# Performance work log

Hardware: AMD Instinct MI355X
Metric: run time of the kernel (lower is better)

Reference implementation:

```python
import jax, jax.numpy as jnp
import numpy as np

T, B, D, H = 1024, 4, 1024, 16
HD = D // H  # 64


def _layernorm(x, g, b, eps=1e-5):
    mu = jnp.mean(x, axis=-1, keepdims=True)
    var = jnp.var(x, axis=-1, keepdims=True)
    return (x - mu) / jnp.sqrt(var + eps) * g + b


def setup_inputs() -> dict:
    key = jax.random.key(0)
    ks = jax.random.split(key, 16)
    s = 1.0 / np.sqrt(D)
    mk = lambda k: jax.random.uniform(k, (D, D), jnp.float32, -s, s)
    return {
        "x": jax.random.normal(ks[0], (T, B, D), jnp.float32),
        "Wq": mk(ks[1]), "bq": jnp.zeros((D,), jnp.float32),
        "Wk": mk(ks[2]), "bk": jnp.zeros((D,), jnp.float32),
        "Wv": mk(ks[3]), "bv": jnp.zeros((D,), jnp.float32),
        "Wo": mk(ks[4]), "bo": jnp.zeros((D,), jnp.float32),
        "Wl": mk(ks[5]), "bl": jnp.zeros((D,), jnp.float32),
        "g1": jnp.ones((D,), jnp.float32), "b1": jnp.zeros((D,), jnp.float32),
        "g2": jnp.ones((D,), jnp.float32), "b2": jnp.zeros((D,), jnp.float32),
    }


def reference(x, Wq, bq, Wk, bk, Wv, bv, Wo, bo, Wl, bl, g1, b1, g2, b2):
    # x: [T, B, D] (time-major). The torch loop over dim 0 with full keys/values
    # is equivalent to batched full (non-causal) self-attention.
    q = (x @ Wq.T + bq).reshape(T, B, H, HD)
    k = (x @ Wk.T + bk).reshape(T, B, H, HD)
    v = (x @ Wv.T + bv).reshape(T, B, H, HD)
    scores = jnp.einsum("tbhd,sbhd->bhts", q, k) / np.sqrt(HD).astype(np.float32)
    attn = jax.nn.softmax(scores, axis=-1)          # [B,H,T,T]
    ctx = jnp.einsum("bhts,sbhd->tbhd", attn, v).reshape(T, B, D)
    attn_out = ctx @ Wo.T + bo
    # dropout p: identity at inference
    h = _layernorm(attn_out + x, g1, b1)
    ffn = h @ Wl.T + bl
    return _layernorm(ffn + h, g2, b2)
```

## Files before the change

### kernel.cpp

```cpp
#include <hip/hip_runtime.h>

#define T_ 1024
#define B_ 4
#define D_ 1024
#define H_ 16
#define HD_ 64
#define M_ (T_ * B_)

typedef _Float16 f16;
typedef f16 f16x8 __attribute__((ext_vector_type(8)));
typedef f16 f16x4 __attribute__((ext_vector_type(4)));
typedef float f32x4 __attribute__((ext_vector_type(4)));

__device__ __forceinline__ void gl2lds16(const void* g, void* l) {
  __builtin_amdgcn_global_load_lds(
      (const __attribute__((address_space(1))) void*)g,
      (__attribute__((address_space(3))) void*)l, 16, 0, 0);
}

struct Prep {
  const float* x;
  const float* w[5];
  const float* b[3];
  f16* xd;
  f16* wd[5];
  float* bd;
};

__global__ __launch_bounds__(256) void prep(Prep p) {
  const int bid = blockIdx.x, tid = threadIdx.x;
  if (bid < 4096) {
    const int i = bid * 1024 + tid * 4;
    float4 v = *(const float4*)(p.x + i);
    f16x4 o = {(f16)v.x, (f16)v.y, (f16)v.z, (f16)v.w};
    *(f16x4*)(p.xd + i) = o;
  } else if (bid < 9216) {
    const int wi = bid - 4096;
    const int a = wi >> 10;
    const int i = (wi & 1023) * 1024 + tid * 4;
    float4 v = *(const float4*)(p.w[a] + i);
    f16x4 o = {(f16)v.x, (f16)v.y, (f16)v.z, (f16)v.w};
    *(f16x4*)(p.wd[a] + i) = o;
  } else {
    const int j = bid - 9216;
    const int i = tid * 4;
    *(float4*)(p.bd + j * 1024 + i) = *(const float4*)(p.b[j] + i);
  }
}

__global__ __launch_bounds__(256) void gemm_f16(const f16* __restrict__ A,
                                                const f16* __restrict__ W,
                                                const float* __restrict__ bias,
                                                const f16* __restrict__ res,
                                                f16* __restrict__ out) {
  constexpr int K = D_, BK = 32;
  __shared__ __align__(16) f16 As[128 * BK];
  __shared__ __align__(16) f16 Bs[64 * BK];
  const int tid = threadIdx.x;
  const int lane = tid & 63;
  const int quad = lane >> 4, l16 = lane & 15;
  const int m0 = blockIdx.y * 128, n0 = blockIdx.x * 64;
  const int wave = tid >> 6;
  const int wm = (wave >> 1) * 64, wn = (wave & 1) * 32;
  f32x4 acc[4][2] = {};
  for (int kt = 0; kt < K / BK; ++kt) {
    __syncthreads();
    const int kb = kt * BK;
#pragma unroll
    for (int i = 0; i < 2; ++i) {
      const int c = i * 256 + tid;
      const int row = c >> 2, col8 = (c & 3) * 8;
      const int ldsbase = (i * 256 + (tid & ~63)) * 8;
      gl2lds16(A + (size_t)(m0 + row) * K + kb + col8, &As[ldsbase]);
    }
    {
      const int row = tid >> 2, col8 = (tid & 3) * 8;
      const int ldsbase = (tid & ~63) * 8;
      gl2lds16(W + (size_t)(n0 + row) * K + kb + col8, &Bs[ldsbase]);
    }
    __syncthreads();
    f16x8 af[4], bf[2];
#pragma unroll
    for (int i = 0; i < 4; ++i)
      af[i] = *(const f16x8*)&As[(wm + i * 16 + l16) * BK + quad * 8];
#pragma unroll
    for (int j = 0; j < 2; ++j)
      bf[j] = *(const f16x8*)&Bs[(wn + j * 16 + l16) * BK + quad * 8];
#pragma unroll
    for (int i = 0; i < 4; ++i)
#pragma unroll
      for (int j = 0; j < 2; ++j)
        acc[i][j] = __builtin_amdgcn_mfma_f32_16x16x32_f16(af[i], bf[j], acc[i][j], 0, 0, 0);
  }
#pragma unroll
  for (int j = 0; j < 2; ++j) {
    const int n = n0 + wn + j * 16 + l16;
    const float bn = bias[n];
#pragma unroll
    for (int i = 0; i < 4; ++i) {
      const int m = m0 + wm + i * 16 + quad * 4;
#pragma unroll
      for (int r = 0; r < 4; ++r) {
        const float v = acc[i][j][r] + bn + (float)res[(size_t)(m + r) * D_ + n];
        out[(size_t)(m + r) * D_ + n] = (f16)v;
      }
    }
  }
}

#define QSCALE 0.18033688011112042f
__global__ __launch_bounds__(256) void gemm_qkv(const f16* __restrict__ A,
                                                const f16* __restrict__ W,
                                                const float* __restrict__ bias,
                                                f16* __restrict__ qo,
                                                f16* __restrict__ ko,
                                                f16* __restrict__ vo) {
  constexpr int K = D_, BK = 32;
  __shared__ __align__(16) f16 As[128 * BK];
  __shared__ __align__(16) f16 Bs[128 * BK];
  const int tid = threadIdx.x;
  const int lane = tid & 63;
  const int quad = lane >> 4, l16 = lane & 15;
  const int m0 = blockIdx.y * 128, n0 = blockIdx.x * 128;
  const int wave = tid >> 6;
  const int wm = (wave >> 1) * 64, wn = (wave & 1) * 64;
  f32x4 acc[4][4] = {};
  for (int kt = 0; kt < K / BK; ++kt) {
    __syncthreads();
    const int kb = kt * BK;
#pragma unroll
    for (int i = 0; i < 2; ++i) {
      const int c = i * 256 + tid;
      const int row = c >> 2, col8 = (c & 3) * 8;
      const int ldsbase = (i * 256 + (tid & ~63)) * 8;
      gl2lds16(A + (size_t)(m0 + row) * K + kb + col8, &As[ldsbase]);
      gl2lds16(W + (size_t)(n0 + row) * K + kb + col8, &Bs[ldsbase]);
    }
    __syncthreads();
    f16x8 af[4], bf[4];
#pragma unroll
    for (int i = 0; i < 4; ++i)
      af[i] = *(const f16x8*)&As[(wm + i * 16 + l16) * BK + quad * 8];
#pragma unroll
    for (int j = 0; j < 4; ++j)
      bf[j] = *(const f16x8*)&Bs[(wn + j * 16 + l16) * BK + quad * 8];
#pragma unroll
    for (int i = 0; i < 4; ++i)
#pragma unroll
      for (int j = 0; j < 4; ++j)
        acc[i][j] = __builtin_amdgcn_mfma_f32_16x16x32_f16(af[i], bf[j], acc[i][j], 0, 0, 0);
  }
  const int which = n0 >> 10;
  f16* outp = which == 0 ? qo : (which == 1 ? ko : vo);
  const float sc = which == 0 ? QSCALE : 1.0f;
#pragma unroll
  for (int j = 0; j < 4; ++j) {
    const int n = n0 + wn + j * 16 + l16;
    const float bn = bias[n];
    const int nl = n & 1023;
    const int hh = nl >> 6, d = nl & 63;
#pragma unroll
    for (int i = 0; i < 4; ++i) {
#pragma unroll
      for (int r = 0; r < 4; ++r) {
        const int m = m0 + wm + i * 16 + quad * 4 + r;
        const float v = (acc[i][j][r] + bn) * sc;
        const int t = m >> 2, bb = m & 3;
        if (which < 2)
          outp[((size_t)(bb * H_ + hh) * T_ + t) * HD_ + d] = (f16)v;
        else
          outp[((size_t)(bb * H_ + hh) * HD_ + d) * T_ + t] = (f16)v;
      }
    }
  }
}

__global__ __launch_bounds__(256) void attn(const f16* __restrict__ Q,
                                            const f16* __restrict__ Km,
                                            const f16* __restrict__ Vt,
                                            f16* __restrict__ ctx) {
  constexpr int SK = 128;
  constexpr int NT = T_ / SK;
  __shared__ __align__(16) f16 Ks[SK * HD_];
  __shared__ __align__(16) f16 Vs[HD_ * SK];
  __shared__ __align__(16) f16 Ps[4][16 * 36];
  const int tid = threadIdx.x, wave = tid >> 6, lane = tid & 63;
  const int quad = lane >> 4, l16 = lane & 15;
  const int bh = blockIdx.x;
  const int b = bh >> 4, h = bh & 15;
  const int q0 = blockIdx.y * 128;
  const f16* Qbh = Q + ((size_t)bh * T_ + q0 + wave * 32) * HD_;
  const f16* Kbh = Km + (size_t)bh * T_ * HD_;
  const f16* Vbh = Vt + (size_t)bh * HD_ * T_;

  f16x8 qf[2][2];
#pragma unroll
  for (int c = 0; c < 2; ++c) {
    qf[c][0] = *(const f16x8*)&Qbh[(c * 16 + l16) * HD_ + quad * 8];
    qf[c][1] = *(const f16x8*)&Qbh[(c * 16 + l16) * HD_ + 32 + quad * 8];
  }

  const f16* kq[4];
  const f16* vq[4];
  int lds_o[4];
#pragma unroll
  for (int it = 0; it < 4; ++it) {
    const int n = wave * 256 + it * 64 + lane;
    const int s = n >> 3, cp = n & 7, cl = cp ^ (s & 7);
    kq[it] = Kbh + (size_t)s * HD_ + cl * 8;
    const int d = n >> 4, cp2 = n & 15, cl2 = cp2 ^ (d & 7);
    vq[it] = Vbh + (size_t)d * T_ + cl2 * 8;
    lds_o[it] = (wave * 256 + it * 64) * 8;
  }

  f32x4 O[4][2] = {};
  float lsum[2] = {0.f, 0.f};
  const int sw = l16 & 7;

  for (int kt = 0; kt < NT; ++kt) {
    __syncthreads();
#pragma unroll
    for (int it = 0; it < 4; ++it) {
      gl2lds16(kq[it], &Ks[lds_o[it]]);
      kq[it] += SK * HD_;
    }
#pragma unroll
    for (int it = 0; it < 4; ++it) {
      gl2lds16(vq[it], &Vs[lds_o[it]]);
      vq[it] += SK;
    }
    __syncthreads();

    float st[8][2][4];
#pragma unroll
    for (int s = 0; s < 8; ++s) {
      const int row = s * 16 + l16;
      const f16x8 ka = *(const f16x8*)&Ks[row * HD_ + (quad ^ sw) * 8];
      const f16x8 kb = *(const f16x8*)&Ks[row * HD_ + ((4 + quad) ^ sw) * 8];
#pragma unroll
      for (int c = 0; c < 2; ++c) {
        f32x4 a = {};
        a = __builtin_amdgcn_mfma_f32_16x16x32_f16(ka, qf[c][0], a, 0, 0, 0);
        a = __builtin_amdgcn_mfma_f32_16x16x32_f16(kb, qf[c][1], a, 0, 0, 0);
#pragma unroll
        for (int r = 0; r < 4; ++r) {
          st[s][c][r] = exp2f(a[r]);
          lsum[c] += st[s][c][r];
        }
      }
    }

#pragma unroll
    for (int cI = 0; cI < 4; ++cI) {
#pragma unroll
      for (int c = 0; c < 2; ++c) {
        f16* pw = &Ps[wave][0];
        f16x4 w0, w1;
#pragma unroll
        for (int r = 0; r < 4; ++r) {
          w0[r] = (f16)st[2 * cI][c][r];
          w1[r] = (f16)st[2 * cI + 1][c][r];
        }
        *(f16x4*)&pw[l16 * 36 + quad * 4] = w0;
        *(f16x4*)&pw[l16 * 36 + 16 + quad * 4] = w1;
        const f16x8 pf = *(const f16x8*)&pw[l16 * 36 + quad * 8];
#pragma unroll
        for (int dt = 0; dt < 4; ++dt) {
          const int d = dt * 16 + l16;
          const f16x8 vf = *(const f16x8*)&Vs[d * SK + (((cI * 4 + quad) ^ sw) * 8)];
          O[dt][c] = __builtin_amdgcn_mfma_f32_16x16x32_f16(vf, pf, O[dt][c], 0, 0, 0);
        }
      }
    }
  }

#pragma unroll
  for (int c = 0; c < 2; ++c) {
    float l = lsum[c];
    l += __shfl_xor(l, 16, 64);
    l += __shfl_xor(l, 32, 64);
    const float linv = 1.f / l;
    const int t = q0 + wave * 32 + c * 16 + l16;
#pragma unroll
    for (int dt = 0; dt < 4; ++dt) {
      f16x4 ov;
#pragma unroll
      for (int r = 0; r < 4; ++r) ov[r] = (f16)(O[dt][c][r] * linv);
      *(f16x4*)&ctx[((size_t)t * B_ + b) * D_ + h * HD_ + dt * 16 + quad * 4] = ov;
    }
  }
}

__global__ __launch_bounds__(256) void lnorm(const f16* __restrict__ a,
                                             const float* __restrict__ g,
                                             const float* __restrict__ bb,
                                             f16* __restrict__ outh,
                                             float* __restrict__ outf) {
  const int row = blockIdx.x, tid = threadIdx.x;
  const size_t base = (size_t)row * D_;
  f16x4 va = *(const f16x4*)&a[base + tid * 4];
  float x0 = (float)va[0], x1 = (float)va[1], x2 = (float)va[2], x3 = (float)va[3];
  float s = x0 + x1 + x2 + x3;
  float sq = x0 * x0 + x1 * x1 + x2 * x2 + x3 * x3;
#pragma unroll
  for (int off = 32; off; off >>= 1) {
    s += __shfl_down(s, off, 64);
    sq += __shfl_down(sq, off, 64);
  }
  __shared__ float rs[4], rq[4];
  __shared__ float mean_s, rstd_s;
  if ((tid & 63) == 0) { rs[tid >> 6] = s; rq[tid >> 6] = sq; }
  __syncthreads();
  if (tid == 0) {
    float S = rs[0] + rs[1] + rs[2] + rs[3];
    float Qq = rq[0] + rq[1] + rq[2] + rq[3];
    float mean = S / D_;
    float var = Qq / D_ - mean * mean;
    mean_s = mean;
    rstd_s = rsqrtf(var + 1e-5f);
  }
  __syncthreads();
  const float mean = mean_s, rstd = rstd_s;
  float4 vg = *(const float4*)&g[tid * 4];
  float4 vb = *(const float4*)&bb[tid * 4];
  float y0 = (x0 - mean) * rstd * vg.x + vb.x;
  float y1 = (x1 - mean) * rstd * vg.y + vb.y;
  float y2 = (x2 - mean) * rstd * vg.z + vb.z;
  float y3 = (x3 - mean) * rstd * vg.w + vb.w;
  if (outh) {
    f16x4 o = {(f16)y0, (f16)y1, (f16)y2, (f16)y3};
    *(f16x4*)&outh[base + tid * 4] = o;
  }
  if (outf)
    *(float4*)&outf[base + tid * 4] = make_float4(y0, y1, y2, y3);
}

extern "C" void kernel_launch(void* const* d_in, const int* in_sizes, int n_in,
                              void* d_out, int out_size, void* d_ws, size_t ws_size,
                              hipStream_t stream) {
  const float* x  = (const float*)d_in[0];
  const float* Wq = (const float*)d_in[1];
  const float* bq = (const float*)d_in[2];
  const float* Wk = (const float*)d_in[3];
  const float* bk = (const float*)d_in[4];
  const float* Wv = (const float*)d_in[5];
  const float* bv = (const float*)d_in[6];
  const float* Wo = (const float*)d_in[7];
  const float* bo = (const float*)d_in[8];
  const float* Wl = (const float*)d_in[9];
  const float* bl = (const float*)d_in[10];
  const float* g1 = (const float*)d_in[11];
  const float* b1 = (const float*)d_in[12];
  const float* g2 = (const float*)d_in[13];
  const float* b2 = (const float*)d_in[14];

  char* ws = (char*)d_ws;
  const size_t MB = 1 << 20;
  f16*   xb   = (f16*)(ws + 0 * MB);
  f16*   wqkv = (f16*)(ws + 8 * MB);
  f16*   wob  = (f16*)(ws + 14 * MB);
  f16*   wlb  = (f16*)(ws + 16 * MB);
  float* bqkv = (float*)(ws + 18 * MB);
  f16*   qb   = (f16*)(ws + 19 * MB);
  f16*   kb   = (f16*)(ws + 27 * MB);
  f16*   vb   = (f16*)(ws + 35 * MB);
  f16*   ctxb = (f16*)(ws + 43 * MB);
  f16*   att  = qb;
  f16*   hbuf = kb;

  Prep p;
  p.x = x;
  p.w[0] = Wq; p.w[1] = Wk; p.w[2] = Wv; p.w[3] = Wo; p.w[4] = Wl;
  p.b[0] = bq; p.b[1] = bk; p.b[2] = bv;
  p.xd = xb;
  p.wd[0] = wqkv; p.wd[1] = wqkv + D_ * D_; p.wd[2] = wqkv + 2 * D_ * D_;
  p.wd[3] = wob; p.wd[4] = wlb;
  p.bd = bqkv;
  prep<<<9219, 256, 0, stream>>>(p);

  gemm_qkv<<<dim3(3 * D_ / 128, M_ / 128), 256, 0, stream>>>(xb, wqkv, bqkv, qb, kb, vb);

  attn<<<dim3(B_ * H_, T_ / 128), 256, 0, stream>>>(qb, kb, vb, ctxb);

  dim3 gg(D_ / 64, M_ / 128);
  gemm_f16<<<gg, 256, 0, stream>>>(ctxb, wob, bo, xb, att);
  lnorm<<<M_, 256, 0, stream>>>(att, g1, b1, hbuf, nullptr);
  gemm_f16<<<gg, 256, 0, stream>>>(hbuf, wlb, bl, hbuf, att);
  lnorm<<<M_, 256, 0, stream>>>(att, g2, b2, nullptr, (float*)d_out);
}
```

Measured before the change: 238.8 us.

## Fuse all stages into one persistent megakernel with grid-wide barriers

```diff
diff --git a/kernel.cpp b/kernel.cpp
--- a/kernel.cpp
+++ b/kernel.cpp
@@ -6,63 +6,94 @@
 #define H_ 16
 #define HD_ 64
 #define M_ (T_ * B_)
+#define NBLK 512
 
 typedef _Float16 f16;
 typedef f16 f16x8 __attribute__((ext_vector_type(8)));
 typedef f16 f16x4 __attribute__((ext_vector_type(4)));
 typedef float f32x4 __attribute__((ext_vector_type(4)));
 
+#define QSCALE 0.18033688011112042f
+
 __device__ __forceinline__ void gl2lds16(const void* g, void* l) {
   __builtin_amdgcn_global_load_lds(
       (const __attribute__((address_space(1))) void*)g,
       (__attribute__((address_space(3))) void*)l, 16, 0, 0);
 }
 
-struct Prep {
+__device__ __forceinline__ void gbar(unsigned* cnt, unsigned* gen) {
+  __syncthreads();
+  if (threadIdx.x == 0) {
+    unsigned g = __hip_atomic_load(gen, __ATOMIC_RELAXED, __HIP_MEMORY_SCOPE_AGENT);
+    __threadfence();
+    unsigned a = __hip_atomic_fetch_add(cnt, 1u, __ATOMIC_ACQ_REL, __HIP_MEMORY_SCOPE_AGENT);
+    if (a == NBLK - 1) {
+      __hip_atomic_store(cnt, 0u, __ATOMIC_RELAXED, __HIP_MEMORY_SCOPE_AGENT);
+      __hip_atomic_fetch_add(gen, 1u, __ATOMIC_RELEASE, __HIP_MEMORY_SCOPE_AGENT);
+    } else {
+      while (__hip_atomic_load(gen, __ATOMIC_ACQUIRE, __HIP_MEMORY_SCOPE_AGENT) == g)
+        __builtin_amdgcn_s_sleep(2);
+    }
+    __threadfence();
+  }
+  __syncthreads();
+}
+
+struct MegaArgs {
   const float* x;
   const float* w[5];
-  const float* b[3];
-  f16* xd;
+  const float* b3[3];
+  const float* bo;
+  const float* bl;
+  const float *g1, *b1, *g2, *b2;
+  f16* xb;
   f16* wd[5];
-  float* bd;
+  float* bqkv;
+  f16 *qb, *kb, *vb, *ctxb, *att, *hbuf;
+  float* out;
+  unsigned* bar;
 };
 
-__global__ __launch_bounds__(256) void prep(Prep p) {
-  const int bid = blockIdx.x, tid = threadIdx.x;
-  if (bid < 4096) {
-    const int i = bid * 1024 + tid * 4;
-    float4 v = *(const float4*)(p.x + i);
+__device__ __forceinline__ void prep_stage(const MegaArgs& A, int gtid) {
+  constexpr int XCH = 1 << 20;
+  constexpr int WCH = 1 << 18;
+  constexpr int NCH = XCH + 5 * WCH;
+#pragma unroll 1
+  for (int i = gtid; i < NCH; i += NBLK * 256) {
+    const float4* s;
+    f16* d;
+    int off;
+    if (i < XCH) {
+      s = (const float4*)A.x; d = A.xb; off = i;
+    } else {
+      const int wi = i - XCH;
+      const int a = wi >> 18;
+      off = wi & (WCH - 1);
+      s = (const float4*)A.w[a];
+      d = A.wd[a];
+    }
+    float4 v = s[off];
     f16x4 o = {(f16)v.x, (f16)v.y, (f16)v.z, (f16)v.w};
-    *(f16x4*)(p.xd + i) = o;
-  } else if (bid < 9216) {
-    const int wi = bid - 4096;
-    const int a = wi >> 10;
-    const int i = (wi & 1023) * 1024 + tid * 4;
-    float4 v = *(const float4*)(p.w[a] + i);
-    f16x4 o = {(f16)v.x, (f16)v.y, (f16)v.z, (f16)v.w};
-    *(f16x4*)(p.wd[a] + i) = o;
-  } else {
-    const int j = bid - 9216;
-    const int i = tid * 4;
-    *(float4*)(p.bd + j * 1024 + i) = *(const float4*)(p.b[j] + i);
-  }
-}
-
-__global__ __launch_bounds__(256) void gemm_f16(const f16* __restrict__ A,
-                                                const f16* __restrict__ W,
-                                                const float* __restrict__ bias,
-                                                const f16* __restrict__ res,
-                                                f16* __restrict__ out) {
+    *(f16x4*)(d + off * 4) = o;
+  }
+  if (gtid < 768) {
+    const int j = gtid >> 8, t = gtid & 255;
+    ((float4*)(A.bqkv + j * 1024))[t] = ((const float4*)A.b3[j])[t];
+  }
+}
+
+__device__ __forceinline__ void qkv_stage(const MegaArgs& A, char* smem, int vt, int tid) {
   constexpr int K = D_, BK = 32;
-  __shared__ __align__(16) f16 As[128 * BK];
-  __shared__ __align__(16) f16 Bs[64 * BK];
-  const int tid = threadIdx.x;
+  f16* As = (f16*)smem;
+  f16* Bs = (f16*)(smem + 8192);
   const int lane = tid & 63;
   const int quad = lane >> 4, l16 = lane & 15;
-  const int m0 = blockIdx.y * 128, n0 = blockIdx.x * 64;
+  const int m0 = (vt / 24) * 128, n0 = (vt % 24) * 128;
   const int wave = tid >> 6;
-  const int wm = (wave >> 1) * 64, wn = (wave & 1) * 32;
-  f32x4 acc[4][2] = {};
+  const int wm = (wave >> 1) * 64, wn = (wave & 1) * 64;
+  const f16* Ap = A.xb;
+  const f16* Wp = A.wd[0];
+  f32x4 acc[4][4] = {};
   for (int kt = 0; kt < K / BK; ++kt) {
     __syncthreads();
     const int kb = kt * BK;
@@ -71,77 +102,15 @@
       const int c = i * 256 + tid;
       const int row = c >> 2, col8 = (c & 3) * 8;
       const int ldsbase = (i * 256 + (tid & ~63)) * 8;
-      gl2lds16(A + (size_t)(m0 + row) * K + kb + col8, &As[ldsbase]);
-    }
-    {
-      const int row = tid >> 2, col8 = (tid & 3) * 8;
-      const int ldsbase = (tid & ~63) * 8;
-      gl2lds16(W + (size_t)(n0 + row) * K + kb + col8, &Bs[ldsbase]);
-    }
-    __syncthreads();
-    f16x8 af[4], bf[2];
+      gl2lds16(Ap + (size_t)(m0 + row) * K + kb + col8, &As[ldsbase]);
+      gl2lds16(Wp + (size_t)(n0 + row) * K + kb + col8, &Bs[ldsbase]);
+    }
+    __syncthreads();
+    f16x8 af[4], bf[4];
 #pragma unroll
     for (int i = 0; i < 4; ++i)
       af[i] = *(const f16x8*)&As[(wm + i * 16 + l16) * BK + quad * 8];
 #pragma unroll
-    for (int j = 0; j < 2; ++j)
-      bf[j] = *(const f16x8*)&Bs[(wn + j * 16 + l16) * BK + quad * 8];
-#pragma unroll
-    for (int i = 0; i < 4; ++i)
-#pragma unroll
-      for (int j = 0; j < 2; ++j)
-        acc[i][j] = __builtin_amdgcn_mfma_f32_16x16x32_f16(af[i], bf[j], acc[i][j], 0, 0, 0);
-  }
-#pragma unroll
-  for (int j = 0; j < 2; ++j) {
-    const int n = n0 + wn + j * 16 + l16;
-    const float bn = bias[n];
-#pragma unroll
-    for (int i = 0; i < 4; ++i) {
-      const int m = m0 + wm + i * 16 + quad * 4;
-#pragma unroll
-      for (int r = 0; r < 4; ++r) {
-        const float v = acc[i][j][r] + bn + (float)res[(size_t)(m + r) * D_ + n];
-        out[(size_t)(m + r) * D_ + n] = (f16)v;
-      }
-    }
-  }
-}
-
-#define QSCALE 0.18033688011112042f
-__global__ __launch_bounds__(256) void gemm_qkv(const f16* __restrict__ A,
-                                                const f16* __restrict__ W,
-                                                const float* __restrict__ bias,
-                                                f16* __restrict__ qo,
-                                                f16* __restrict__ ko,
-                                                f16* __restrict__ vo) {
-  constexpr int K = D_, BK = 32;
-  __shared__ __align__(16) f16 As[128 * BK];
-  __shared__ __align__(16) f16 Bs[128 * BK];
-  const int tid = threadIdx.x;
-  const int lane = tid & 63;
-  const int quad = lane >> 4, l16 = lane & 15;
-  const int m0 = blockIdx.y * 128, n0 = blockIdx.x * 128;
-  const int wave = tid >> 6;
-  const int wm = (wave >> 1) * 64, wn = (wave & 1) * 64;
-  f32x4 acc[4][4] = {};
-  for (int kt = 0; kt < K / BK; ++kt) {
-    __syncthreads();
-    const int kb = kt * BK;
-#pragma unroll
-    for (int i = 0; i < 2; ++i) {
-      const int c = i * 256 + tid;
-      const int row = c >> 2, col8 = (c & 3) * 8;
-      const int ldsbase = (i * 256 + (tid & ~63)) * 8;
-      gl2lds16(A + (size_t)(m0 + row) * K + kb + col8, &As[ldsbase]);
-      gl2lds16(W + (size_t)(n0 + row) * K + kb + col8, &Bs[ldsbase]);
-    }
-    __syncthreads();
-    f16x8 af[4], bf[4];
-#pragma unroll
-    for (int i = 0; i < 4; ++i)
-      af[i] = *(const f16x8*)&As[(wm + i * 16 + l16) * BK + quad * 8];
-#pragma unroll
     for (int j = 0; j < 4; ++j)
       bf[j] = *(const f16x8*)&Bs[(wn + j * 16 + l16) * BK + quad * 8];
 #pragma unroll
@@ -151,12 +120,12 @@
         acc[i][j] = __builtin_amdgcn_mfma_f32_16x16x32_f16(af[i], bf[j], acc[i][j], 0, 0, 0);
   }
   const int which = n0 >> 10;
-  f16* outp = which == 0 ? qo : (which == 1 ? ko : vo);
+  f16* outp = which == 0 ? A.qb : (which == 1 ? A.kb : A.vb);
   const float sc = which == 0 ? QSCALE : 1.0f;
 #pragma unroll
   for (int j = 0; j < 4; ++j) {
     const int n = n0 + wn + j * 16 + l16;
-    const float bn = bias[n];
+    const float bn = A.bqkv[n];
     const int nl = n & 1023;
     const int hh = nl >> 6, d = nl & 63;
 #pragma unroll
@@ -175,23 +144,20 @@
   }
 }
 
-__global__ __launch_bounds__(256) void attn(const f16* __restrict__ Q,
-                                            const f16* __restrict__ Km,
-                                            const f16* __restrict__ Vt,
-                                            f16* __restrict__ ctx) {
+__device__ __forceinline__ void attn_stage(const MegaArgs& A, char* smem, int vt, int tid) {
   constexpr int SK = 128;
   constexpr int NT = T_ / SK;
-  __shared__ __align__(16) f16 Ks[SK * HD_];
-  __shared__ __align__(16) f16 Vs[HD_ * SK];
-  __shared__ __align__(16) f16 Ps[4][16 * 36];
-  const int tid = threadIdx.x, wave = tid >> 6, lane = tid & 63;
+  f16* Ks = (f16*)smem;
+  f16* Vs = (f16*)(smem + 16384);
+  f16* Psb = (f16*)smem;
+  const int wave = tid >> 6, lane = tid & 63;
   const int quad = lane >> 4, l16 = lane & 15;
-  const int bh = blockIdx.x;
+  const int bh = vt & 63;
   const int b = bh >> 4, h = bh & 15;
-  const int q0 = blockIdx.y * 128;
-  const f16* Qbh = Q + ((size_t)bh * T_ + q0 + wave * 32) * HD_;
-  const f16* Kbh = Km + (size_t)bh * T_ * HD_;
-  const f16* Vbh = Vt + (size_t)bh * HD_ * T_;
+  const int q0 = (vt >> 6) * 128;
+  const f16* Qbh = A.qb + ((size_t)bh * T_ + q0 + wave * 32) * HD_;
+  const f16* Kbh = A.kb + (size_t)bh * T_ * HD_;
+  const f16* Vbh = A.vb + (size_t)bh * HD_ * T_;
 
   f16x8 qf[2][2];
 #pragma unroll
@@ -249,12 +215,13 @@
         }
       }
     }
+    __syncthreads();
 
 #pragma unroll
     for (int cI = 0; cI < 4; ++cI) {
 #pragma unroll
       for (int c = 0; c < 2; ++c) {
-        f16* pw = &Ps[wave][0];
+        f16* pw = &Psb[wave * 16 * 36];
         f16x4 w0, w1;
 #pragma unroll
         for (int r = 0; r < 4; ++r) {
@@ -286,17 +253,78 @@
       f16x4 ov;
 #pragma unroll
       for (int r = 0; r < 4; ++r) ov[r] = (f16)(O[dt][c][r] * linv);
-      *(f16x4*)&ctx[((size_t)t * B_ + b) * D_ + h * HD_ + dt * 16 + quad * 4] = ov;
-    }
-  }
-}
-
-__global__ __launch_bounds__(256) void lnorm(const f16* __restrict__ a,
-                                             const float* __restrict__ g,
-                                             const float* __restrict__ bb,
-                                             f16* __restrict__ outh,
-                                             float* __restrict__ outf) {
-  const int row = blockIdx.x, tid = threadIdx.x;
+      *(f16x4*)&A.ctxb[((size_t)t * B_ + b) * D_ + h * HD_ + dt * 16 + quad * 4] = ov;
+    }
+  }
+}
+
+__device__ __forceinline__ void gemm_stage(const f16* __restrict__ Ap,
+                                           const f16* __restrict__ Wp,
+                                           const float* __restrict__ bias,
+                                           const f16* __restrict__ res,
+                                           f16* __restrict__ out,
+                                           char* smem, int vt, int tid) {
+  constexpr int K = D_, BK = 32;
+  f16* As = (f16*)smem;
+  f16* Bs = (f16*)(smem + 8192);
+  const int lane = tid & 63;
+  const int quad = lane >> 4, l16 = lane & 15;
+  const int m0 = (vt / 16) * 128, n0 = (vt % 16) * 64;
+  const int wave = tid >> 6;
+  const int wm = (wave >> 1) * 64, wn = (wave & 1) * 32;
+  f32x4 acc[4][2] = {};
+  for (int kt = 0; kt < K / BK; ++kt) {
+    __syncthreads();
+    const int kb = kt * BK;
+#pragma unroll
+    for (int i = 0; i < 2; ++i) {
+      const int c = i * 256 + tid;
+      const int row = c >> 2, col8 = (c & 3) * 8;
+      const int ldsbase = (i * 256 + (tid & ~63)) * 8;
+      gl2lds16(Ap + (size_t)(m0 + row) * K + kb + col8, &As[ldsbase]);
+    }
+    {
+      const int row = tid >> 2, col8 = (tid & 3) * 8;
+      const int ldsbase = (tid & ~63) * 8;
+      gl2lds16(Wp + (size_t)(n0 + row) * K + kb + col8, &Bs[ldsbase]);
+    }
+    __syncthreads();
+    f16x8 af[4], bf[2];
+#pragma unroll
+    for (int i = 0; i < 4; ++i)
+      af[i] = *(const f16x8*)&As[(wm + i * 16 + l16) * BK + quad * 8];
+#pragma unroll
+    for (int j = 0; j < 2; ++j)
+      bf[j] = *(const f16x8*)&Bs[(wn + j * 16 + l16) * BK + quad * 8];
+#pragma unroll
+    for (int i = 0; i < 4; ++i)
+#pragma unroll
+      for (int j = 0; j < 2; ++j)
+        acc[i][j] = __builtin_amdgcn_mfma_f32_16x16x32_f16(af[i], bf[j], acc[i][j], 0, 0, 0);
+  }
+#pragma unroll
+  for (int j = 0; j < 2; ++j) {
+    const int n = n0 + wn + j * 16 + l16;
+    const float bn = bias[n];
+#pragma unroll
+    for (int i = 0; i < 4; ++i) {
+      const int m = m0 + wm + i * 16 + quad * 4;
+#pragma unroll
+      for (int r = 0; r < 4; ++r) {
+        const float v = acc[i][j][r] + bn + (float)res[(size_t)(m + r) * D_ + n];
+        out[(size_t)(m + r) * D_ + n] = (f16)v;
+      }
+    }
+  }
+}
+
+__device__ __forceinline__ void lnorm_stage(const f16* __restrict__ a,
+                                            const float* __restrict__ g,
+                                            const float* __restrict__ bb,
+                                            f16* __restrict__ outh,
+                                            float* __restrict__ outf,
+                                            char* smem, int row, int tid) {
+  float* sc = (float*)smem;
   const size_t base = (size_t)row * D_;
   f16x4 va = *(const f16x4*)&a[base + tid * 4];
   float x0 = (float)va[0], x1 = (float)va[1], x2 = (float)va[2], x3 = (float)va[3];
@@ -307,20 +335,19 @@
     s += __shfl_down(s, off, 64);
     sq += __shfl_down(sq, off, 64);
   }
-  __shared__ float rs[4], rq[4];
-  __shared__ float mean_s, rstd_s;
-  if ((tid & 63) == 0) { rs[tid >> 6] = s; rq[tid >> 6] = sq; }
+  if ((tid & 63) == 0) { sc[tid >> 6] = s; sc[8 + (tid >> 6)] = sq; }
   __syncthreads();
   if (tid == 0) {
-    float S = rs[0] + rs[1] + rs[2] + rs[3];
-    float Qq = rq[0] + rq[1] + rq[2] + rq[3];
+    float S = sc[0] + sc[1] + sc[2] + sc[3];
+    float Qq = sc[8] + sc[9] + sc[10] + sc[11];
     float mean = S / D_;
     float var = Qq / D_ - mean * mean;
-    mean_s = mean;
-    rstd_s = rsqrtf(var + 1e-5f);
+    sc[16] = mean;
+    sc[17] = rsqrtf(var + 1e-5f);
   }
   __syncthreads();
-  const float mean = mean_s, rstd = rstd_s;
+  const float mean = sc[16], rstd = sc[17];
+  __syncthreads();
   float4 vg = *(const float4*)&g[tid * 4];
   float4 vb = *(const float4*)&bb[tid * 4];
   float y0 = (x0 - mean) * rstd * vg.x + vb.x;
@@ -335,25 +362,42 @@
     *(float4*)&outf[base + tid * 4] = make_float4(y0, y1, y2, y3);
 }
 
+__global__ __launch_bounds__(256, 2) void mega(MegaArgs A) {
+  __shared__ __align__(16) char smem[32768];
+  const int bid = blockIdx.x, tid = threadIdx.x;
+  const int gtid = bid * 256 + tid;
+  unsigned* cnt = A.bar;
+  unsigned* gen = A.bar + 1;
+
+  prep_stage(A, gtid);
+  gbar(cnt, gen);
+
+#pragma unroll 1
+  for (int vt = bid; vt < 768; vt += NBLK) qkv_stage(A, smem, vt, tid);
+  gbar(cnt, gen);
+
+  attn_stage(A, smem, bid, tid);
+  gbar(cnt, gen);
+
+  gemm_stage(A.ctxb, A.wd[3], A.bo, A.xb, A.att, smem, bid, tid);
+  gbar(cnt, gen);
+
+#pragma unroll 1
+  for (int r = bid * 8; r < bid * 8 + 8; ++r)
+    lnorm_stage(A.att, A.g1, A.b1, A.hbuf, nullptr, smem, r, tid);
+  gbar(cnt, gen);
+
+  gemm_stage(A.hbuf, A.wd[4], A.bl, A.hbuf, A.att, smem, bid, tid);
+  gbar(cnt, gen);
+
+#pragma unroll 1
+  for (int r = bid * 8; r < bid * 8 + 8; ++r)
+    lnorm_stage(A.att, A.g2, A.b2, nullptr, A.out, smem, r, tid);
+}
+
 extern "C" void kernel_launch(void* const* d_in, const int* in_sizes, int n_in,
                               void* d_out, int out_size, void* d_ws, size_t ws_size,
                               hipStream_t stream) {
-  const float* x  = (const float*)d_in[0];
-  const float* Wq = (const float*)d_in[1];
-  const float* bq = (const float*)d_in[2];
-  const float* Wk = (const float*)d_in[3];
-  const float* bk = (const float*)d_in[4];
-  const float* Wv = (const float*)d_in[5];
-  const float* bv = (const float*)d_in[6];
-  const float* Wo = (const float*)d_in[7];
-  const float* bo = (const float*)d_in[8];
-  const float* Wl = (const float*)d_in[9];
-  const float* bl = (const float*)d_in[10];
-  const float* g1 = (const float*)d_in[11];
-  const float* b1 = (const float*)d_in[12];
-  const float* g2 = (const float*)d_in[13];
-  const float* b2 = (const float*)d_in[14];
-
   char* ws = (char*)d_ws;
   const size_t MB = 1 << 20;
   f16*   xb   = (f16*)(ws + 0 * MB);
@@ -365,26 +409,37 @@
   f16*   kb   = (f16*)(ws + 27 * MB);
   f16*   vb   = (f16*)(ws + 35 * MB);
   f16*   ctxb = (f16*)(ws + 43 * MB);
-  f16*   att  = qb;
-  f16*   hbuf = kb;
-
-  Prep p;
-  p.x = x;
-  p.w[0] = Wq; p.w[1] = Wk; p.w[2] = Wv; p.w[3] = Wo; p.w[4] = Wl;
-  p.b[0] = bq; p.b[1] = bk; p.b[2] = bv;
-  p.xd = xb;
-  p.wd[0] = wqkv; p.wd[1] = wqkv + D_ * D_; p.wd[2] = wqkv + 2 * D_ * D_;
-  p.wd[3] = wob; p.wd[4] = wlb;
-  p.bd = bqkv;
-  prep<<<9219, 256, 0, stream>>>(p);
-
-  gemm_qkv<<<dim3(3 * D_ / 128, M_ / 128), 256, 0, stream>>>(xb, wqkv, bqkv, qb, kb, vb);
-
-  attn<<<dim3(B_ * H_, T_ / 128), 256, 0, stream>>>(qb, kb, vb, ctxb);
-
-  dim3 gg(D_ / 64, M_ / 128);
-  gemm_f16<<<gg, 256, 0, stream>>>(ctxb, wob, bo, xb, att);
-  lnorm<<<M_, 256, 0, stream>>>(att, g1, b1, hbuf, nullptr);
-  gemm_f16<<<gg, 256, 0, stream>>>(hbuf, wlb, bl, hbuf, att);
-  lnorm<<<M_, 256, 0, stream>>>(att, g2, b2, nullptr, (float*)d_out);
-}
+  unsigned* bar = (unsigned*)(ws + 51 * MB);
+
+  MegaArgs ma;
+  ma.x = (const float*)d_in[0];
+  ma.w[0] = (const float*)d_in[1];
+  ma.b3[0] = (const float*)d_in[2];
+  ma.w[1] = (const float*)d_in[3];
+  ma.b3[1] = (const float*)d_in[4];
+  ma.w[2] = (const float*)d_in[5];
+  ma.b3[2] = (const float*)d_in[6];
+  ma.w[3] = (const float*)d_in[7];
+  ma.bo = (const float*)d_in[8];
+  ma.w[4] = (const float*)d_in[9];
+  ma.bl = (const float*)d_in[10];
+  ma.g1 = (const float*)d_in[11];
+  ma.b1 = (const float*)d_in[12];
+  ma.g2 = (const float*)d_in[13];
+  ma.b2 = (const float*)d_in[14];
+  ma.xb = xb;
+  ma.wd[0] = wqkv;
+  ma.wd[1] = wqkv + D_ * D_;
+  ma.wd[2] = wqkv + 2 * D_ * D_;
+  ma.wd[3] = wob;
+  ma.wd[4] = wlb;
+  ma.bqkv = bqkv;
+  ma.qb = qb; ma.kb = kb; ma.vb = vb; ma.ctxb = ctxb;
+  ma.att = qb;
+  ma.hbuf = kb;
+  ma.out = (float*)d_out;
+  ma.bar = bar;
+
+  hipMemsetAsync(bar, 0, 128, stream);
+  mega<<<NBLK, 256, 0, stream>>>(ma);
+}
```

New measurement: 850.7 us. 256% more time.
